# Optimization experiments

Measured on AMD Instinct MI355X. Metric: run time of the kernel, lower is better.

The kernel has to match this reference:

```python
import jax, jax.numpy as jnp
import numpy as np

NUM_LAYERS = 3

def setup_inputs() -> dict:
    key = jax.random.key(0)
    ks = jax.random.split(key, 16)
    B = 8192
    NU, NI, D = 60000, 40000, 64
    N = NU + NI
    T_TRAIN, T_MAX = 128, 256
    E = 1600000
    return {
        "user_indices": jax.random.randint(ks[0], (B,), 0, NU, dtype=jnp.int32).astype(jnp.int64),
        "item_indices": jax.random.randint(ks[1], (B,), 0, NI, dtype=jnp.int32).astype(jnp.int64),
        "time_diffs": jax.random.randint(ks[2], (B,), 0, T_TRAIN, dtype=jnp.int32).astype(jnp.int64),
        "user_trends": jax.random.normal(ks[3], (B, T_TRAIN), dtype=jnp.float32),
        "item_trends": jax.random.normal(ks[4], (B, T_TRAIN), dtype=jnp.float32),
        "user_emb_table": 0.01 * jax.random.normal(ks[5], (NU, D), dtype=jnp.float32),
        "item_emb_table": 0.01 * jax.random.normal(ks[6], (NI, D), dtype=jnp.float32),
        "user_time_table": 0.01 * jax.random.normal(ks[7], (NU, T_MAX), dtype=jnp.float32),
        "item_time_table": 0.01 * jax.random.normal(ks[8], (NI, T_MAX), dtype=jnp.float32),
        "W1": 0.05 * jax.random.normal(ks[9], (T_TRAIN, 32), dtype=jnp.float32),
        "b1": jnp.zeros((32,), dtype=jnp.float32),
        "W2": 0.05 * jax.random.normal(ks[10], (32, T_MAX - T_TRAIN), dtype=jnp.float32),
        "b2": jnp.zeros((T_MAX - T_TRAIN,), dtype=jnp.float32),
        "edge_src": jax.random.randint(ks[11], (E,), 0, N, dtype=jnp.int32),
        "edge_dst": jax.random.randint(ks[12], (E,), 0, N, dtype=jnp.int32),
    }


def _graph_forward(user_emb_table, item_emb_table, edge_src, edge_dst):
    # LightGCN-style: mean of in-neighbor source features, num_layers hops,
    # then average over [input, layer1, ..., layerL] embeddings.
    N = user_emb_table.shape[0] + item_emb_table.shape[0]
    emb = jnp.concatenate([user_emb_table, item_emb_table], axis=0)  # [N, D]
    deg = jax.ops.segment_sum(jnp.ones_like(edge_dst, dtype=emb.dtype), edge_dst, num_segments=N)
    inv_deg = jnp.where(deg > 0, 1.0 / jnp.maximum(deg, 1.0), 0.0)[:, None]  # zero for isolated nodes (DGL mean -> 0)
    acc = emb
    cur = emb
    for _ in range(NUM_LAYERS):
        msgs = cur[edge_src]  # [E, D] gather
        summed = jax.ops.segment_sum(msgs, edge_dst, num_segments=N)
        cur = summed * inv_deg
        acc = acc + cur
    final = acc / jnp.asarray(NUM_LAYERS + 1, emb.dtype)
    return final[: user_emb_table.shape[0]], final[user_emb_table.shape[0]:]


def _mlp(t, W1, b1, W2, b2):
    # Linear->ReLU->Dropout(eval: identity)->Linear
    h = jax.nn.relu(t @ W1 + b1)
    return h @ W2 + b2


def reference(user_indices, item_indices, time_diffs, user_trends, item_trends,
              user_emb_table, item_emb_table, user_time_table, item_time_table,
              W1, b1, W2, b2, edge_src, edge_dst):
    user_embeddings, item_embeddings = _graph_forward(user_emb_table, item_emb_table, edge_src, edge_dst)
    ue = user_embeddings[user_indices]  # [B, D]
    ie = item_embeddings[item_indices]  # [B, D]
    global_match = jnp.sum(ue * ie, axis=-1)  # [B]

    ute = user_time_table[user_indices]  # [B, T_MAX]
    ite = item_time_table[item_indices]
    ut = jnp.concatenate([user_trends, _mlp(user_trends, W1, b1, W2, b2)], axis=1)  # [B, T_MAX]
    it = jnp.concatenate([item_trends, _mlp(item_trends, W1, b1, W2, b2)], axis=1)
    user_time_match = jnp.sum(ute * ut, axis=-1)
    item_time_match = jnp.sum(ite * it, axis=-1)

    B = user_indices.shape[0]
    ue0 = user_emb_table[user_indices]
    ie0 = item_emb_table[item_indices]
    reg_loss = 0.5 * (jnp.sum(ue0 ** 2) + jnp.sum(ie0 ** 2) + jnp.sum(ute ** 2) + jnp.sum(ite ** 2)) / float(B)

    return (jax.nn.sigmoid(global_match), jax.nn.sigmoid(user_time_match + item_time_match), reg_loss)
```

## Files before the change

### kernel.cpp

```cpp
#include <hip/hip_runtime.h>
#include <math.h>


__device__ __forceinline__ float bf2f(unsigned short h) {
    return __uint_as_float((unsigned)h << 16);
}
__device__ __forceinline__ unsigned short f2bf(float f) {
    unsigned u = __float_as_uint(f);
    return (unsigned short)((u + 0x7fffu + ((u >> 16) & 1u)) >> 16);
}


__global__ __launch_bounds__(256) void conv_kernel(
    const float* __restrict__ utab, const float* __restrict__ itab,
    unsigned short* __restrict__ fb, int total, int uElems,
    int* __restrict__ cursor2, int convBlocks) {
    int bid = blockIdx.x;
    if (bid == convBlocks) {
        cursor2[threadIdx.x] = 0;
        return;
    }
    int i = (bid * 256 + threadIdx.x) * 4;
    if (i >= total + 64) return;
    ushort4 o;
    if (i < total) {
        const float* srcp = (i < uElems) ? (utab + i) : (itab + (i - uElems));
        float4 v = *(const float4*)srcp;
        o.x = f2bf(v.x); o.y = f2bf(v.y); o.z = f2bf(v.z); o.w = f2bf(v.w);
    } else {
        o.x = 0; o.y = 0; o.z = 0; o.w = 0;
    }
    *(ushort4*)(fb + i) = o;
}


__global__ __launch_bounds__(256) void bin2_kernel(
    const int* __restrict__ src, const int* __restrict__ dst,
    int* __restrict__ cursor2, unsigned long long* __restrict__ pairs2,
    int E, int cap) {
    __shared__ int lcnt[256];
    __shared__ int lbase[256];
    int tid = threadIdx.x;
    int base = blockIdx.x * 4096;
    lcnt[tid] = 0;
    __syncthreads();
    #pragma unroll
    for (int i = 0; i < 16; ++i) {
        int e = base + i * 256 + tid;
        if (e < E) atomicAdd(&lcnt[dst[e] >> 9], 1);
    }
    __syncthreads();
    int c = lcnt[tid];
    lbase[tid] = (c > 0) ? atomicAdd(&cursor2[tid], c) : 0;
    __syncthreads();
    lcnt[tid] = 0;
    __syncthreads();
    #pragma unroll
    for (int i = 0; i < 16; ++i) {
        int e = base + i * 256 + tid;
        if (e < E) {
            int d = dst[e], s = src[e];
            int b = d >> 9;
            int r = lbase[b] + atomicAdd(&lcnt[b], 1);
            if (r < cap)
                pairs2[(size_t)b * cap + r] =
                    ((unsigned long long)(unsigned)d << 32) | (unsigned)s;
        }
    }
}


__global__ __launch_bounds__(256) void sort3_kernel(
    const unsigned long long* __restrict__ pairs2,
    const int* __restrict__ cursor2,
    float* __restrict__ invd, int* __restrict__ csr, int NODE_N, int cap) {
    __shared__ int lcnt[512];
    int bin = blockIdx.x;
    int nodebase = bin << 9;
    int n = cursor2[bin];
    if (n > cap) n = cap;
    const unsigned long long* p = pairs2 + (size_t)bin * cap;
    int tid = threadIdx.x;

    lcnt[tid] = 0;
    lcnt[tid + 256] = 0;
    __syncthreads();
    for (int i = tid; i < n; i += 256) {
        unsigned long long pr = p[i];
        int d = (int)(pr >> 32), s = (int)(pr & 0xffffffffu);
        int pos = atomicAdd(&lcnt[d - nodebase], 1);
        if (pos < 64) csr[(size_t)d * 64 + pos] = s;
    }
    __syncthreads();
    #pragma unroll
    for (int t = 0; t < 2; ++t) {
        int j = tid + t * 256;
        int node = nodebase + j;
        if (node <= NODE_N) {
            int own = lcnt[j];
            invd[node] = (own > 0) ? 1.0f / (float)own : 0.0f;
            int d0 = (own < 64) ? own : 64;
            int pend = (own <= 32) ? 32 : 64;
            int* row = csr + (size_t)node * 64;
            for (int k = d0; k < pend; ++k) row[k] = NODE_N;
        }
    }
}


#define GATHER4(buf, sv, gx, gy, gz, gw_)                                  \
    {                                                                      \
        ushort4 v_ = *(const ushort4*)((buf) + (size_t)(sv) * 64 + 4 * cL);\
        gx += bf2f(v_.x); gy += bf2f(v_.y);                                \
        gz += bf2f(v_.z); gw_ += bf2f(v_.w);                               \
    }
#define RED2(x) { x += __shfl_xor(x, 16, 64); x += __shfl_xor(x, 32, 64); }

__global__ __launch_bounds__(256) void prop_kernel(
    const unsigned short* __restrict__ cur,
    const int* __restrict__ csr, const float* __restrict__ invd,
    unsigned short* __restrict__ nxt, int NP1) {
    int w = (blockIdx.x * blockDim.x + threadIdx.x) >> 6;
    int lane = threadIdx.x & 63;
    int n0 = 2 * w, n1 = 2 * w + 1;
    if (n0 >= NP1) return;
    bool v1 = (n1 < NP1);
    int n1c = v1 ? n1 : n0;
    int g = lane >> 4;
    int cL = lane & 15;
    const int* c0 = csr + (size_t)n0 * 64;
    const int* c1 = csr + (size_t)n1c * 64;
    float inv0 = invd[n0];
    float inv1 = v1 ? invd[n1c] : 0.f;
    int s0 = c0[g], s1 = c0[4 + g], s2 = c0[8 + g], s3 = c0[12 + g];
    int t0 = c1[g], t1 = c1[4 + g], t2 = c1[8 + g], t3 = c1[12 + g];

    float ax = 0.f, ay = 0.f, az = 0.f, aw = 0.f;
    float bx = 0.f, by = 0.f, bz = 0.f, bw = 0.f;
    float ex = 0.f, ey = 0.f, ez = 0.f, ew = 0.f;
    float fx = 0.f, fy = 0.f, fz = 0.f, fw = 0.f;
    GATHER4(cur, s0, ax, ay, az, aw);
    GATHER4(cur, s1, bx, by, bz, bw);
    GATHER4(cur, t0, ex, ey, ez, ew);
    GATHER4(cur, t1, fx, fy, fz, fw);
    GATHER4(cur, s2, ax, ay, az, aw);
    GATHER4(cur, s3, bx, by, bz, bw);
    GATHER4(cur, t2, ex, ey, ez, ew);
    GATHER4(cur, t3, fx, fy, fz, fw);

    int deg0 = (inv0 > 0.f) ? (int)(1.0f / inv0 + 0.5f) : 0;
    int deg1 = (inv1 > 0.f) ? (int)(1.0f / inv1 + 0.5f) : 0;
    if (deg0 > 16) {
        int s4 = c0[16 + g], s5 = c0[20 + g], s6 = c0[24 + g], s7 = c0[28 + g];
        GATHER4(cur, s4, ax, ay, az, aw);
        GATHER4(cur, s5, bx, by, bz, bw);
        GATHER4(cur, s6, ax, ay, az, aw);
        GATHER4(cur, s7, bx, by, bz, bw);
    }
    if (deg1 > 16) {
        int t4 = c1[16 + g], t5 = c1[20 + g], t6 = c1[24 + g], t7 = c1[28 + g];
        GATHER4(cur, t4, ex, ey, ez, ew);
        GATHER4(cur, t5, fx, fy, fz, fw);
        GATHER4(cur, t6, ex, ey, ez, ew);
        GATHER4(cur, t7, fx, fy, fz, fw);
    }
    if (deg0 > 32) {
        #pragma unroll
        for (int pb = 32; pb < 64; pb += 8) {
            int u0 = c0[pb + g], u1 = c0[pb + 4 + g];
            GATHER4(cur, u0, ax, ay, az, aw);
            GATHER4(cur, u1, bx, by, bz, bw);
        }
    }
    if (deg1 > 32) {
        #pragma unroll
        for (int pb = 32; pb < 64; pb += 8) {
            int u0 = c1[pb + g], u1 = c1[pb + 4 + g];
            GATHER4(cur, u0, ex, ey, ez, ew);
            GATHER4(cur, u1, fx, fy, fz, fw);
        }
    }
    ax += bx; ay += by; az += bz; aw += bw;
    ex += fx; ey += fy; ez += fz; ew += fw;
    RED2(ax); RED2(ay); RED2(az); RED2(aw);
    RED2(ex); RED2(ey); RED2(ez); RED2(ew);
    if (g == 0) {
        ushort4 o;
        o.x = f2bf(ax * inv0); o.y = f2bf(ay * inv0);
        o.z = f2bf(az * inv0); o.w = f2bf(aw * inv0);
        *(ushort4*)(nxt + (size_t)n0 * 64 + 4 * cL) = o;
    } else if (g == 1 && v1) {
        ushort4 o;
        o.x = f2bf(ex * inv1); o.y = f2bf(ey * inv1);
        o.z = f2bf(ez * inv1); o.w = f2bf(ew * inv1);
        *(ushort4*)(nxt + (size_t)n1c * 64 + 4 * cL) = o;
    }
}


__global__ __launch_bounds__(256) void match_kernel(
    const int* __restrict__ uidx, const int* __restrict__ iidx,
    const float* __restrict__ utr, const float* __restrict__ itr,
    const float* __restrict__ utt, const float* __restrict__ itt,
    const float* __restrict__ utab, const float* __restrict__ itab,
    const float* __restrict__ W1, const float* __restrict__ b1,
    const float* __restrict__ W2, const float* __restrict__ b2,
    float* __restrict__ out1, float* __restrict__ regpart, int B) {
    __shared__ float sh[4][320];
    __shared__ float rsh[4];
    int wid = threadIdx.x >> 6, lane = threadIdx.x & 63;
    int b = blockIdx.x * 4 + wid;
    bool valid = (b < B);
    int bb = valid ? b : (B - 1);
    int u = uidx[bb], it = iidx[bb];

    const float* uterow = utt + (size_t)u * 256;
    const float* iterow = itt + (size_t)it * 256;
    float ute0 = uterow[lane], ute1 = uterow[64 + lane], ute2 = uterow[128 + lane], ute3 = uterow[192 + lane];
    float ite0 = iterow[lane], ite1 = iterow[64 + lane], ite2 = iterow[128 + lane], ite3 = iterow[192 + lane];
    float ue0 = utab[(size_t)u * 64 + lane], ie0 = itab[(size_t)it * 64 + lane];
    float tu0 = utr[(size_t)bb * 128 + lane], tu1 = utr[(size_t)bb * 128 + 64 + lane];
    float ti0 = itr[(size_t)bb * 128 + lane], ti1 = itr[(size_t)bb * 128 + 64 + lane];

    float* tu = sh[wid];
    float* ti = tu + 128;
    float* hu = ti + 128;
    float* hi = hu + 32;
    tu[lane] = tu0; tu[lane + 64] = tu1;
    ti[lane] = ti0; ti[lane + 64] = ti1;
    __syncthreads();

    {
        int j = lane & 31;
        const float* t = (lane < 32) ? tu : ti;
        float a0 = b1[j], a1 = 0.f, a2 = 0.f, a3 = 0.f;
        #pragma unroll
        for (int k = 0; k < 128; k += 4) {
            a0 += t[k]     * W1[k * 32 + j];
            a1 += t[k + 1] * W1[(k + 1) * 32 + j];
            a2 += t[k + 2] * W1[(k + 2) * 32 + j];
            a3 += t[k + 3] * W1[(k + 3) * 32 + j];
        }
        float* h = (lane < 32) ? hu : hi;
        h[j] = fmaxf((a0 + a1) + (a2 + a3), 0.0f);
    }
    __syncthreads();

    float mu0 = b2[lane], mu1 = b2[64 + lane];
    float mi0 = b2[lane], mi1 = b2[64 + lane];
    #pragma unroll 8
    for (int j = 0; j < 32; ++j) {
        float w0 = W2[j * 128 + lane], w1 = W2[j * 128 + 64 + lane];
        float huj = hu[j], hij = hi[j];
        mu0 += huj * w0; mu1 += huj * w1;
        mi0 += hij * w0; mi1 += hij * w1;
    }

    float utm = ute0 * tu0 + ute1 * tu1 + ute2 * mu0 + ute3 * mu1;
    float itm = ite0 * ti0 + ite1 * ti1 + ite2 * mi0 + ite3 * mi1;

    float reg = ute0 * ute0 + ute1 * ute1 + ute2 * ute2 + ute3 * ute3
              + ite0 * ite0 + ite1 * ite1 + ite2 * ite2 + ite3 * ite3
              + ue0 * ue0 + ie0 * ie0;

    float s = utm + itm;
    for (int o = 32; o; o >>= 1) {
        s   += __shfl_down(s, o, 64);
        reg += __shfl_down(reg, o, 64);
    }
    if (lane == 0) {
        if (valid) out1[b] = 1.0f / (1.0f + expf(-s));
        rsh[wid] = valid ? reg : 0.0f;
    }
    __syncthreads();
    if (threadIdx.x == 0)
        regpart[blockIdx.x] = rsh[0] + rsh[1] + rsh[2] + rsh[3];
}


__global__ __launch_bounds__(256) void gdot_kernel(
    const int* __restrict__ uidx, const int* __restrict__ iidx,
    const unsigned short* __restrict__ fb2,
    const unsigned short* __restrict__ fb1l,
    const int* __restrict__ csr, const float* __restrict__ invd,
    const float* __restrict__ utab, const float* __restrict__ itab,
    float* __restrict__ out0, const float* __restrict__ regpart,
    float* __restrict__ out2, int B, int NU, int gBlocks, int nReg,
    float regScale) {
    if ((int)blockIdx.x == gBlocks) {
        __shared__ float sh[256];
        float s = 0.0f;
        for (int i = threadIdx.x; i < nReg; i += 256) s += regpart[i];
        sh[threadIdx.x] = s;
        __syncthreads();
        for (int o = 128; o; o >>= 1) {
            if (threadIdx.x < (unsigned)o) sh[threadIdx.x] += sh[threadIdx.x + o];
            __syncthreads();
        }
        if (threadIdx.x == 0) out2[0] = sh[0] * regScale;
        return;
    }
    int wid = threadIdx.x >> 6, lane = threadIdx.x & 63;
    int b = blockIdx.x * 4 + wid;
    if (b >= B) return;
    int g = lane >> 4;
    int cL = lane & 15;
    int u = uidx[b], it = iidx[b];
    int nodeU = u, nodeI = NU + it;
    const int* cu = csr + (size_t)nodeU * 64;
    const int* ci = csr + (size_t)nodeI * 64;
    float invU = invd[nodeU];
    float invI = invd[nodeI];
    float4 l0u = *(const float4*)(utab + (size_t)nodeU * 64 + 4 * cL);
    float4 l0i = *(const float4*)(itab + (size_t)it * 64 + 4 * cL);
    ushort4 l1u = *(const ushort4*)(fb1l + (size_t)nodeU * 64 + 4 * cL);
    ushort4 l1i = *(const ushort4*)(fb1l + (size_t)nodeI * 64 + 4 * cL);
    ushort4 l2u = *(const ushort4*)(fb2 + (size_t)nodeU * 64 + 4 * cL);
    ushort4 l2i = *(const ushort4*)(fb2 + (size_t)nodeI * 64 + 4 * cL);
    int s0 = cu[g],      s1 = cu[4 + g],  s2 = cu[8 + g],  s3 = cu[12 + g];
    int s4 = cu[16 + g], s5 = cu[20 + g], s6 = cu[24 + g], s7 = cu[28 + g];
    int t0 = ci[g],      t1 = ci[4 + g],  t2 = ci[8 + g],  t3 = ci[12 + g];
    int t4 = ci[16 + g], t5 = ci[20 + g], t6 = ci[24 + g], t7 = ci[28 + g];

    float ax = 0.f, ay = 0.f, az = 0.f, aw = 0.f;
    float bx = 0.f, by = 0.f, bz = 0.f, bw = 0.f;
    float ex = 0.f, ey = 0.f, ez = 0.f, ew = 0.f;
    float fx = 0.f, fy = 0.f, fz = 0.f, fw = 0.f;
    GATHER4(fb2, s0, ax, ay, az, aw);
    GATHER4(fb2, s1, bx, by, bz, bw);
    GATHER4(fb2, t0, ex, ey, ez, ew);
    GATHER4(fb2, t1, fx, fy, fz, fw);
    GATHER4(fb2, s2, ax, ay, az, aw);
    GATHER4(fb2, s3, bx, by, bz, bw);
    GATHER4(fb2, t2, ex, ey, ez, ew);
    GATHER4(fb2, t3, fx, fy, fz, fw);
    GATHER4(fb2, s4, ax, ay, az, aw);
    GATHER4(fb2, s5, bx, by, bz, bw);
    GATHER4(fb2, t4, ex, ey, ez, ew);
    GATHER4(fb2, t5, fx, fy, fz, fw);
    GATHER4(fb2, s6, ax, ay, az, aw);
    GATHER4(fb2, s7, bx, by, bz, bw);
    GATHER4(fb2, t6, ex, ey, ez, ew);
    GATHER4(fb2, t7, fx, fy, fz, fw);

    int degU = (invU > 0.f) ? (int)(1.0f / invU + 0.5f) : 0;
    int degI = (invI > 0.f) ? (int)(1.0f / invI + 0.5f) : 0;
    if (degU > 32) {
        #pragma unroll
        for (int pb = 32; pb < 64; pb += 8) {
            int u0 = cu[pb + g], u1 = cu[pb + 4 + g];
            GATHER4(fb2, u0, ax, ay, az, aw);
            GATHER4(fb2, u1, bx, by, bz, bw);
        }
    }
    if (degI > 32) {
        #pragma unroll
        for (int pb = 32; pb < 64; pb += 8) {
            int u0 = ci[pb + g], u1 = ci[pb + 4 + g];
            GATHER4(fb2, u0, ex, ey, ez, ew);
            GATHER4(fb2, u1, fx, fy, fz, fw);
        }
    }
    ax += bx; ay += by; az += bz; aw += bw;
    ex += fx; ey += fy; ez += fz; ew += fw;
    RED2(ax); RED2(ay); RED2(az); RED2(aw);
    RED2(ex); RED2(ey); RED2(ez); RED2(ew);

    float ue0_ = l0u.x + bf2f(l1u.x) + bf2f(l2u.x) + ax * invU;
    float ue1_ = l0u.y + bf2f(l1u.y) + bf2f(l2u.y) + ay * invU;
    float ue2_ = l0u.z + bf2f(l1u.z) + bf2f(l2u.z) + az * invU;
    float ue3_ = l0u.w + bf2f(l1u.w) + bf2f(l2u.w) + aw * invU;
    float ie0_ = l0i.x + bf2f(l1i.x) + bf2f(l2i.x) + ex * invI;
    float ie1_ = l0i.y + bf2f(l1i.y) + bf2f(l2i.y) + ey * invI;
    float ie2_ = l0i.z + bf2f(l1i.z) + bf2f(l2i.z) + ez * invI;
    float ie3_ = l0i.w + bf2f(l1i.w) + bf2f(l2i.w) + ew * invI;

    float dv = ue0_ * ie0_ + ue1_ * ie1_ + ue2_ * ie2_ + ue3_ * ie3_;
    for (int o = 32; o; o >>= 1) dv += __shfl_down(dv, o, 64);
    if (lane == 0)
        out0[b] = 1.0f / (1.0f + expf(-dv * (1.0f / 64.0f)));
}

extern "C" void kernel_launch(void* const* d_in, const int* in_sizes, int n_in,
                              void* d_out, int out_size, void* d_ws, size_t ws_size,
                              hipStream_t stream) {
    const int*   uidx = (const int*)d_in[0];
    const int*   iidx = (const int*)d_in[1];
    const float* utr  = (const float*)d_in[3];
    const float* itr  = (const float*)d_in[4];
    const float* utab = (const float*)d_in[5];
    const float* itab = (const float*)d_in[6];
    const float* utt  = (const float*)d_in[7];
    const float* itt  = (const float*)d_in[8];
    const float* W1   = (const float*)d_in[9];
    const float* b1   = (const float*)d_in[10];
    const float* W2   = (const float*)d_in[11];
    const float* b2   = (const float*)d_in[12];
    const int*   esrc = (const int*)d_in[13];
    const int*   edst = (const int*)d_in[14];

    const int B  = in_sizes[0];
    const int H  = in_sizes[10];
    const int TT = in_sizes[9] / H;
    const int TM = TT + in_sizes[12];
    const int NU = in_sizes[7] / TM;
    const int NI = in_sizes[8] / TM;
    const int N  = NU + NI;
    const int E  = in_sizes[13];
    const int D  = 64;
    const int nbin = (N + 1 + 511) >> 9;
    const int cap = 12288;

    char* ws = (char*)d_ws;
    size_t o = 0;
    auto carve = [&](size_t bytes) -> char* {
        char* p = ws + o;
        o = (o + bytes + 255) & ~(size_t)255;
        return p;
    };
    unsigned short* fb0 = (unsigned short*)carve((size_t)(N + 1) * D * sizeof(unsigned short));
    size_t fb1Bytes = (size_t)(N + 1) * D * sizeof(unsigned short);
    size_t p2Bytes  = (size_t)256 * cap * sizeof(unsigned long long);
    unsigned short* fb1 = (unsigned short*)carve(fb1Bytes > p2Bytes ? fb1Bytes : p2Bytes);
    float* invd    = (float*)carve((size_t)(N + 2) * sizeof(float));
    int*   csr     = (int*)  carve((size_t)(N + 1) * 64 * sizeof(int));
    int*   cursor2 = (int*)  carve(256 * sizeof(int));
    float* regpart = (float*)carve((size_t)((B + 3) / 4) * sizeof(float));
    (void)ws_size;

    unsigned long long* pairs2 = (unsigned long long*)fb1;

    float* out0 = (float*)d_out;
    float* out1 = out0 + B;
    float* out2 = out1 + B;

    const int convBlocks = ((N * D + 64) / 4 + 255) / 256;
    conv_kernel<<<convBlocks + 1, 256, 0, stream>>>(
        utab, itab, fb0, N * D, NU * D, cursor2, convBlocks);

    bin2_kernel<<<(E + 4095) / 4096, 256, 0, stream>>>(esrc, edst, cursor2, pairs2, E, cap);
    sort3_kernel<<<nbin, 256, 0, stream>>>(pairs2, cursor2, invd, csr, N, cap);

    const int NP1 = N + 1;
    const int prop_waves = (NP1 + 1) / 2;
    const int prop_blocks = (prop_waves * 64 + 255) / 256;
    prop_kernel<<<prop_blocks, 256, 0, stream>>>(fb0, csr, invd, fb1, NP1);
    prop_kernel<<<prop_blocks, 256, 0, stream>>>(fb1, csr, invd, fb0, NP1);

    const int mBlocks = (B + 3) / 4;
    match_kernel<<<mBlocks, 256, 0, stream>>>(
        uidx, iidx, utr, itr, utt, itt, utab, itab, W1, b1, W2, b2,
        out1, regpart, B);

    const int gBlocks = (B + 3) / 4;
    gdot_kernel<<<gBlocks + 1, 256, 0, stream>>>(
        uidx, iidx, fb0, fb1, csr, invd, utab, itab,
        out0, regpart, out2, B, NU, gBlocks, mBlocks, 0.5f / (float)B);
}
```

Baseline: 142.6 us.

## Fuse match kernel into conversion launch and load CSR rows via shuffles

The separate time-match kernel is folded into the bf16 conversion launch as extra blocks, so one kernel launch goes away and the match work overlaps with the table conversion. In the propagation and final dot kernels, each wave now loads a node's full 64-entry CSR row with one coalesced per-lane load and hands neighbor indices to lanes with __shfl, replacing the repeated scalar loads. This trades memory load instructions for cross-lane shuffles. The fused kernel also grows its shared-memory footprint for the conversion blocks, which may lower their occupancy slightly.

```diff
diff --git a/kernel.cpp b/kernel.cpp
--- a/kernel.cpp
+++ b/kernel.cpp
@@ -10,27 +10,114 @@
     return (unsigned short)((u + 0x7fffu + ((u >> 16) & 1u)) >> 16);
 }
 
-
-__global__ __launch_bounds__(256) void conv_kernel(
+#define GATHER4(buf, sv, gx, gy, gz, gw_)                                  \
+    {                                                                      \
+        ushort4 v_ = *(const ushort4*)((buf) + (size_t)(sv) * 64 + 4 * cL);\
+        gx += bf2f(v_.x); gy += bf2f(v_.y);                                \
+        gz += bf2f(v_.z); gw_ += bf2f(v_.w);                               \
+    }
+#define RED2(x) { x += __shfl_xor(x, 16, 64); x += __shfl_xor(x, 32, 64); }
+
+
+__global__ __launch_bounds__(256) void convmatch_kernel(
     const float* __restrict__ utab, const float* __restrict__ itab,
     unsigned short* __restrict__ fb, int total, int uElems,
-    int* __restrict__ cursor2, int convBlocks) {
+    int* __restrict__ cursor2, int convBlocks,
+    const int* __restrict__ uidx, const int* __restrict__ iidx,
+    const float* __restrict__ utr, const float* __restrict__ itr,
+    const float* __restrict__ utt, const float* __restrict__ itt,
+    const float* __restrict__ W1, const float* __restrict__ b1,
+    const float* __restrict__ W2, const float* __restrict__ b2,
+    float* __restrict__ out1, float* __restrict__ regpart, int B) {
     int bid = blockIdx.x;
+    if (bid < convBlocks) {
+        int i = (bid * 256 + threadIdx.x) * 4;
+        if (i >= total + 64) return;
+        ushort4 o;
+        if (i < total) {
+            const float* srcp = (i < uElems) ? (utab + i) : (itab + (i - uElems));
+            float4 v = *(const float4*)srcp;
+            o.x = f2bf(v.x); o.y = f2bf(v.y); o.z = f2bf(v.z); o.w = f2bf(v.w);
+        } else {
+            o.x = 0; o.y = 0; o.z = 0; o.w = 0;
+        }
+        *(ushort4*)(fb + i) = o;
+        return;
+    }
     if (bid == convBlocks) {
         cursor2[threadIdx.x] = 0;
         return;
     }
-    int i = (bid * 256 + threadIdx.x) * 4;
-    if (i >= total + 64) return;
-    ushort4 o;
-    if (i < total) {
-        const float* srcp = (i < uElems) ? (utab + i) : (itab + (i - uElems));
-        float4 v = *(const float4*)srcp;
-        o.x = f2bf(v.x); o.y = f2bf(v.y); o.z = f2bf(v.z); o.w = f2bf(v.w);
-    } else {
-        o.x = 0; o.y = 0; o.z = 0; o.w = 0;
-    }
-    *(ushort4*)(fb + i) = o;
+    __shared__ float sh[4][320];
+    __shared__ float rsh[4];
+    int mb = bid - convBlocks - 1;
+    int wid = threadIdx.x >> 6, lane = threadIdx.x & 63;
+    int b = mb * 4 + wid;
+    bool valid = (b < B);
+    int bb = valid ? b : (B - 1);
+    int u = uidx[bb], it = iidx[bb];
+
+    const float* uterow = utt + (size_t)u * 256;
+    const float* iterow = itt + (size_t)it * 256;
+    float ute0 = uterow[lane], ute1 = uterow[64 + lane], ute2 = uterow[128 + lane], ute3 = uterow[192 + lane];
+    float ite0 = iterow[lane], ite1 = iterow[64 + lane], ite2 = iterow[128 + lane], ite3 = iterow[192 + lane];
+    float ue0 = utab[(size_t)u * 64 + lane], ie0 = itab[(size_t)it * 64 + lane];
+    float tu0 = utr[(size_t)bb * 128 + lane], tu1 = utr[(size_t)bb * 128 + 64 + lane];
+    float ti0 = itr[(size_t)bb * 128 + lane], ti1 = itr[(size_t)bb * 128 + 64 + lane];
+
+    float* tu = sh[wid];
+    float* ti = tu + 128;
+    float* hu = ti + 128;
+    float* hi = hu + 32;
+    tu[lane] = tu0; tu[lane + 64] = tu1;
+    ti[lane] = ti0; ti[lane + 64] = ti1;
+    __syncthreads();
+
+    {
+        int j = lane & 31;
+        const float* t = (lane < 32) ? tu : ti;
+        float a0 = b1[j], a1 = 0.f, a2 = 0.f, a3 = 0.f;
+        #pragma unroll
+        for (int k = 0; k < 128; k += 4) {
+            a0 += t[k]     * W1[k * 32 + j];
+            a1 += t[k + 1] * W1[(k + 1) * 32 + j];
+            a2 += t[k + 2] * W1[(k + 2) * 32 + j];
+            a3 += t[k + 3] * W1[(k + 3) * 32 + j];
+        }
+        float* h = (lane < 32) ? hu : hi;
+        h[j] = fmaxf((a0 + a1) + (a2 + a3), 0.0f);
+    }
+    __syncthreads();
+
+    float mu0 = b2[lane], mu1 = b2[64 + lane];
+    float mi0 = b2[lane], mi1 = b2[64 + lane];
+    #pragma unroll 8
+    for (int j = 0; j < 32; ++j) {
+        float w0 = W2[j * 128 + lane], w1 = W2[j * 128 + 64 + lane];
+        float huj = hu[j], hij = hi[j];
+        mu0 += huj * w0; mu1 += huj * w1;
+        mi0 += hij * w0; mi1 += hij * w1;
+    }
+
+    float utm = ute0 * tu0 + ute1 * tu1 + ute2 * mu0 + ute3 * mu1;
+    float itm = ite0 * ti0 + ite1 * ti1 + ite2 * mi0 + ite3 * mi1;
+
+    float reg = ute0 * ute0 + ute1 * ute1 + ute2 * ute2 + ute3 * ute3
+              + ite0 * ite0 + ite1 * ite1 + ite2 * ite2 + ite3 * ite3
+              + ue0 * ue0 + ie0 * ie0;
+
+    float s = utm + itm;
+    for (int o = 32; o; o >>= 1) {
+        s   += __shfl_down(s, o, 64);
+        reg += __shfl_down(reg, o, 64);
+    }
+    if (lane == 0) {
+        if (valid) out1[b] = 1.0f / (1.0f + expf(-s));
+        rsh[wid] = valid ? reg : 0.0f;
+    }
+    __syncthreads();
+    if (threadIdx.x == 0)
+        regpart[mb] = rsh[0] + rsh[1] + rsh[2] + rsh[3];
 }
 
 
@@ -107,14 +194,6 @@
     }
 }
 
-
-#define GATHER4(buf, sv, gx, gy, gz, gw_)                                  \
-    {                                                                      \
-        ushort4 v_ = *(const ushort4*)((buf) + (size_t)(sv) * 64 + 4 * cL);\
-        gx += bf2f(v_.x); gy += bf2f(v_.y);                                \
-        gz += bf2f(v_.z); gw_ += bf2f(v_.w);                               \
-    }
-#define RED2(x) { x += __shfl_xor(x, 16, 64); x += __shfl_xor(x, 32, 64); }
 
 __global__ __launch_bounds__(256) void prop_kernel(
     const unsigned short* __restrict__ cur,
@@ -128,12 +207,14 @@
     int n1c = v1 ? n1 : n0;
     int g = lane >> 4;
     int cL = lane & 15;
-    const int* c0 = csr + (size_t)n0 * 64;
-    const int* c1 = csr + (size_t)n1c * 64;
+    int ld0 = csr[(size_t)n0 * 64 + lane];
+    int ld1 = csr[(size_t)n1c * 64 + lane];
     float inv0 = invd[n0];
     float inv1 = v1 ? invd[n1c] : 0.f;
-    int s0 = c0[g], s1 = c0[4 + g], s2 = c0[8 + g], s3 = c0[12 + g];
-    int t0 = c1[g], t1 = c1[4 + g], t2 = c1[8 + g], t3 = c1[12 + g];
+    int s0 = __shfl(ld0, g, 64),      s1 = __shfl(ld0, 4 + g, 64);
+    int s2 = __shfl(ld0, 8 + g, 64),  s3 = __shfl(ld0, 12 + g, 64);
+    int t0 = __shfl(ld1, g, 64),      t1 = __shfl(ld1, 4 + g, 64);
+    int t2 = __shfl(ld1, 8 + g, 64),  t3 = __shfl(ld1, 12 + g, 64);
 
     float ax = 0.f, ay = 0.f, az = 0.f, aw = 0.f;
     float bx = 0.f, by = 0.f, bz = 0.f, bw = 0.f;
@@ -151,14 +232,16 @@
     int deg0 = (inv0 > 0.f) ? (int)(1.0f / inv0 + 0.5f) : 0;
     int deg1 = (inv1 > 0.f) ? (int)(1.0f / inv1 + 0.5f) : 0;
     if (deg0 > 16) {
-        int s4 = c0[16 + g], s5 = c0[20 + g], s6 = c0[24 + g], s7 = c0[28 + g];
+        int s4 = __shfl(ld0, 16 + g, 64), s5 = __shfl(ld0, 20 + g, 64);
+        int s6 = __shfl(ld0, 24 + g, 64), s7 = __shfl(ld0, 28 + g, 64);
         GATHER4(cur, s4, ax, ay, az, aw);
         GATHER4(cur, s5, bx, by, bz, bw);
         GATHER4(cur, s6, ax, ay, az, aw);
         GATHER4(cur, s7, bx, by, bz, bw);
     }
     if (deg1 > 16) {
-        int t4 = c1[16 + g], t5 = c1[20 + g], t6 = c1[24 + g], t7 = c1[28 + g];
+        int t4 = __shfl(ld1, 16 + g, 64), t5 = __shfl(ld1, 20 + g, 64);
+        int t6 = __shfl(ld1, 24 + g, 64), t7 = __shfl(ld1, 28 + g, 64);
         GATHER4(cur, t4, ex, ey, ez, ew);
         GATHER4(cur, t5, fx, fy, fz, fw);
         GATHER4(cur, t6, ex, ey, ez, ew);
@@ -167,7 +250,7 @@
     if (deg0 > 32) {
         #pragma unroll
         for (int pb = 32; pb < 64; pb += 8) {
-            int u0 = c0[pb + g], u1 = c0[pb + 4 + g];
+            int u0 = __shfl(ld0, pb + g, 64), u1 = __shfl(ld0, pb + 4 + g, 64);
             GATHER4(cur, u0, ax, ay, az, aw);
             GATHER4(cur, u1, bx, by, bz, bw);
         }
@@ -175,7 +258,7 @@
     if (deg1 > 32) {
         #pragma unroll
         for (int pb = 32; pb < 64; pb += 8) {
-            int u0 = c1[pb + g], u1 = c1[pb + 4 + g];
+            int u0 = __shfl(ld1, pb + g, 64), u1 = __shfl(ld1, pb + 4 + g, 64);
             GATHER4(cur, u0, ex, ey, ez, ew);
             GATHER4(cur, u1, fx, fy, fz, fw);
         }
@@ -195,86 +278,6 @@
         o.z = f2bf(ez * inv1); o.w = f2bf(ew * inv1);
         *(ushort4*)(nxt + (size_t)n1c * 64 + 4 * cL) = o;
     }
-}
-
-
-__global__ __launch_bounds__(256) void match_kernel(
-    const int* __restrict__ uidx, const int* __restrict__ iidx,
-    const float* __restrict__ utr, const float* __restrict__ itr,
-    const float* __restrict__ utt, const float* __restrict__ itt,
-    const float* __restrict__ utab, const float* __restrict__ itab,
-    const float* __restrict__ W1, const float* __restrict__ b1,
-    const float* __restrict__ W2, const float* __restrict__ b2,
-    float* __restrict__ out1, float* __restrict__ regpart, int B) {
-    __shared__ float sh[4][320];
-    __shared__ float rsh[4];
-    int wid = threadIdx.x >> 6, lane = threadIdx.x & 63;
-    int b = blockIdx.x * 4 + wid;
-    bool valid = (b < B);
-    int bb = valid ? b : (B - 1);
-    int u = uidx[bb], it = iidx[bb];
-
-    const float* uterow = utt + (size_t)u * 256;
-    const float* iterow = itt + (size_t)it * 256;
-    float ute0 = uterow[lane], ute1 = uterow[64 + lane], ute2 = uterow[128 + lane], ute3 = uterow[192 + lane];
-    float ite0 = iterow[lane], ite1 = iterow[64 + lane], ite2 = iterow[128 + lane], ite3 = iterow[192 + lane];
-    float ue0 = utab[(size_t)u * 64 + lane], ie0 = itab[(size_t)it * 64 + lane];
-    float tu0 = utr[(size_t)bb * 128 + lane], tu1 = utr[(size_t)bb * 128 + 64 + lane];
-    float ti0 = itr[(size_t)bb * 128 + lane], ti1 = itr[(size_t)bb * 128 + 64 + lane];
-
-    float* tu = sh[wid];
-    float* ti = tu + 128;
-    float* hu = ti + 128;
-    float* hi = hu + 32;
-    tu[lane] = tu0; tu[lane + 64] = tu1;
-    ti[lane] = ti0; ti[lane + 64] = ti1;
-    __syncthreads();
-
-    {
-        int j = lane & 31;
-        const float* t = (lane < 32) ? tu : ti;
-        float a0 = b1[j], a1 = 0.f, a2 = 0.f, a3 = 0.f;
-        #pragma unroll
-        for (int k = 0; k < 128; k += 4) {
-            a0 += t[k]     * W1[k * 32 + j];
-            a1 += t[k + 1] * W1[(k + 1) * 32 + j];
-            a2 += t[k + 2] * W1[(k + 2) * 32 + j];
-            a3 += t[k + 3] * W1[(k + 3) * 32 + j];
-        }
-        float* h = (lane < 32) ? hu : hi;
-        h[j] = fmaxf((a0 + a1) + (a2 + a3), 0.0f);
-    }
-    __syncthreads();
-
-    float mu0 = b2[lane], mu1 = b2[64 + lane];
-    float mi0 = b2[lane], mi1 = b2[64 + lane];
-    #pragma unroll 8
-    for (int j = 0; j < 32; ++j) {
-        float w0 = W2[j * 128 + lane], w1 = W2[j * 128 + 64 + lane];
-        float huj = hu[j], hij = hi[j];
-        mu0 += huj * w0; mu1 += huj * w1;
-        mi0 += hij * w0; mi1 += hij * w1;
-    }
-
-    float utm = ute0 * tu0 + ute1 * tu1 + ute2 * mu0 + ute3 * mu1;
-    float itm = ite0 * ti0 + ite1 * ti1 + ite2 * mi0 + ite3 * mi1;
-
-    float reg = ute0 * ute0 + ute1 * ute1 + ute2 * ute2 + ute3 * ute3
-              + ite0 * ite0 + ite1 * ite1 + ite2 * ite2 + ite3 * ite3
-              + ue0 * ue0 + ie0 * ie0;
-
-    float s = utm + itm;
-    for (int o = 32; o; o >>= 1) {
-        s   += __shfl_down(s, o, 64);
-        reg += __shfl_down(reg, o, 64);
-    }
-    if (lane == 0) {
-        if (valid) out1[b] = 1.0f / (1.0f + expf(-s));
-        rsh[wid] = valid ? reg : 0.0f;
-    }
-    __syncthreads();
-    if (threadIdx.x == 0)
-        regpart[blockIdx.x] = rsh[0] + rsh[1] + rsh[2] + rsh[3];
 }
 
 
@@ -307,20 +310,25 @@
     int cL = lane & 15;
     int u = uidx[b], it = iidx[b];
     int nodeU = u, nodeI = NU + it;
-    const int* cu = csr + (size_t)nodeU * 64;
-    const int* ci = csr + (size_t)nodeI * 64;
     float invU = invd[nodeU];
     float invI = invd[nodeI];
+    int ldU = csr[(size_t)nodeU * 64 + lane];
+    int ldI = csr[(size_t)nodeI * 64 + lane];
     float4 l0u = *(const float4*)(utab + (size_t)nodeU * 64 + 4 * cL);
     float4 l0i = *(const float4*)(itab + (size_t)it * 64 + 4 * cL);
     ushort4 l1u = *(const ushort4*)(fb1l + (size_t)nodeU * 64 + 4 * cL);
     ushort4 l1i = *(const ushort4*)(fb1l + (size_t)nodeI * 64 + 4 * cL);
     ushort4 l2u = *(const ushort4*)(fb2 + (size_t)nodeU * 64 + 4 * cL);
     ushort4 l2i = *(const ushort4*)(fb2 + (size_t)nodeI * 64 + 4 * cL);
-    int s0 = cu[g],      s1 = cu[4 + g],  s2 = cu[8 + g],  s3 = cu[12 + g];
-    int s4 = cu[16 + g], s5 = cu[20 + g], s6 = cu[24 + g], s7 = cu[28 + g];
-    int t0 = ci[g],      t1 = ci[4 + g],  t2 = ci[8 + g],  t3 = ci[12 + g];
-    int t4 = ci[16 + g], t5 = ci[20 + g], t6 = ci[24 + g], t7 = ci[28 + g];
+
+    int s0 = __shfl(ldU, g, 64),      s1 = __shfl(ldU, 4 + g, 64);
+    int s2 = __shfl(ldU, 8 + g, 64),  s3 = __shfl(ldU, 12 + g, 64);
+    int s4 = __shfl(ldU, 16 + g, 64), s5 = __shfl(ldU, 20 + g, 64);
+    int s6 = __shfl(ldU, 24 + g, 64), s7 = __shfl(ldU, 28 + g, 64);
+    int t0 = __shfl(ldI, g, 64),      t1 = __shfl(ldI, 4 + g, 64);
+    int t2 = __shfl(ldI, 8 + g, 64),  t3 = __shfl(ldI, 12 + g, 64);
+    int t4 = __shfl(ldI, 16 + g, 64), t5 = __shfl(ldI, 20 + g, 64);
+    int t6 = __shfl(ldI, 24 + g, 64), t7 = __shfl(ldI, 28 + g, 64);
 
     float ax = 0.f, ay = 0.f, az = 0.f, aw = 0.f;
     float bx = 0.f, by = 0.f, bz = 0.f, bw = 0.f;
@@ -348,7 +356,7 @@
     if (degU > 32) {
         #pragma unroll
         for (int pb = 32; pb < 64; pb += 8) {
-            int u0 = cu[pb + g], u1 = cu[pb + 4 + g];
+            int u0 = __shfl(ldU, pb + g, 64), u1 = __shfl(ldU, pb + 4 + g, 64);
             GATHER4(fb2, u0, ax, ay, az, aw);
             GATHER4(fb2, u1, bx, by, bz, bw);
         }
@@ -356,7 +364,7 @@
     if (degI > 32) {
         #pragma unroll
         for (int pb = 32; pb < 64; pb += 8) {
-            int u0 = ci[pb + g], u1 = ci[pb + 4 + g];
+            int u0 = __shfl(ldI, pb + g, 64), u1 = __shfl(ldI, pb + 4 + g, 64);
             GATHER4(fb2, u0, ex, ey, ez, ew);
             GATHER4(fb2, u1, fx, fy, fz, fw);
         }
@@ -435,8 +443,10 @@
     float* out2 = out1 + B;
 
     const int convBlocks = ((N * D + 64) / 4 + 255) / 256;
-    conv_kernel<<<convBlocks + 1, 256, 0, stream>>>(
-        utab, itab, fb0, N * D, NU * D, cursor2, convBlocks);
+    const int mBlocks = (B + 3) / 4;
+    convmatch_kernel<<<convBlocks + 1 + mBlocks, 256, 0, stream>>>(
+        utab, itab, fb0, N * D, NU * D, cursor2, convBlocks,
+        uidx, iidx, utr, itr, utt, itt, W1, b1, W2, b2, out1, regpart, B);
 
     bin2_kernel<<<(E + 4095) / 4096, 256, 0, stream>>>(esrc, edst, cursor2, pairs2, E, cap);
     sort3_kernel<<<nbin, 256, 0, stream>>>(pairs2, cursor2, invd, csr, N, cap);
@@ -447,11 +457,6 @@
     prop_kernel<<<prop_blocks, 256, 0, stream>>>(fb0, csr, invd, fb1, NP1);
     prop_kernel<<<prop_blocks, 256, 0, stream>>>(fb1, csr, invd, fb0, NP1);
 
-    const int mBlocks = (B + 3) / 4;
-    match_kernel<<<mBlocks, 256, 0, stream>>>(
-        uidx, iidx, utr, itr, utt, itt, utab, itab, W1, b1, W2, b2,
-        out1, regpart, B);
-
     const int gBlocks = (B + 3) / 4;
     gdot_kernel<<<gBlocks + 1, 256, 0, stream>>>(
         uidx, iidx, fb0, fb1, csr, invd, utab, itab,
```

Result: no change. 144.1 us (+1.0%).
